# Performance work log

Hardware: AMD Instinct MI355X
Metric: run time of the kernel (lower is better)

## Reference

```python
import jax, jax.numpy as jnp
import numpy as np

UNITS = 256   # wiring.units (state size)
OUT = 64      # wiring.output_dim (motor neurons = last OUT units)


def setup_inputs() -> dict:
    key = jax.random.key(0)
    k_x, k_wi, k_wr, k_mi, k_mr = jax.random.split(key, 5)
    B, L, C = 32, 8192, 128
    x = jax.random.normal(k_x, (B, L, C), dtype=jnp.float32)
    # learned parameters
    W_in = jax.random.normal(k_wi, (C, UNITS), dtype=jnp.float32) * 0.05
    W_rec = jax.random.normal(k_wr, (UNITS, UNITS), dtype=jnp.float32) * 0.05
    b = jnp.zeros((UNITS,), dtype=jnp.float32)
    # fixed sparse wiring masks (sensory adjacency [C,U], recurrent adjacency [U,U])
    M_in = jax.random.bernoulli(k_mi, 0.5, (C, UNITS)).astype(jnp.float32)
    M_rec = jax.random.bernoulli(k_mr, 0.5, (UNITS, UNITS)).astype(jnp.float32)
    return {"x": x, "W_in": W_in, "W_rec": W_rec, "b": b, "M_in": M_in, "M_rec": M_rec}


def reference(x, W_in, W_rec, b, M_in, M_rec):
    # Pre-apply the wiring sparsity masks once (original masks weights each step).
    Wi = W_in * M_in          # [C, U]
    Wr = W_rec * M_rec        # [U, U]
    B = x.shape[0]
    h0 = jnp.zeros((B, UNITS), dtype=x.dtype)
    xT = jnp.swapaxes(x, 0, 1)  # [L, B, C] -> scan over time

    def step(h, xt):
        h_new = jnp.tanh(xt @ Wi + h @ Wr + b)   # wired RNN cell, tanh nonlinearity
        # output_size < state_size: emit only motor neurons (last OUT units)
        return h_new, h_new[:, UNITS - OUT:]

    h_last, ys = jax.lax.scan(step, h0, xT)      # ys: [L, B, OUT]
    readout = jnp.swapaxes(ys, 0, 1)             # [B, L, OUT] (batch_first, return_sequences)
    return readout, h_last
```

## Files before the change

### kernel.cpp

```cpp
#include <hip/hip_runtime.h>
#include <hip/hip_bf16.h>
#include <stdint.h>


#define NB 32
#define SL 8192
#define NC 128
#define NU 256
#define NO 64
#define NK 384
#define GR 64
#define TC 16
#define NCHUNK (SL / TC)

typedef _Float16 h16;
typedef __attribute__((ext_vector_type(2))) _Float16 h16x2;

__device__ __forceinline__ float fdot2f(h16x2 a, h16x2 b, float c) {
#if __has_builtin(__builtin_amdgcn_fdot2)
    return __builtin_amdgcn_fdot2(a, b, c, false);
#else
    return c + (float)a[0] * (float)b[0] + (float)a[1] * (float)b[1];
#endif
}

__device__ __forceinline__ float ftanh(float x) {
#if __has_builtin(__builtin_amdgcn_exp2f) && __has_builtin(__builtin_amdgcn_rcpf)
    float e = __builtin_amdgcn_exp2f(x * 2.8853900817779268f);
    return 1.0f - 2.0f * __builtin_amdgcn_rcpf(e + 1.0f);
#else
    return tanhf(x);
#endif
}

__global__ __launch_bounds__(256, 4) void xw_gemm_kernel(
    const float* __restrict__ x,
    const float* __restrict__ W_in,
    const float* __restrict__ bias,
    const float* __restrict__ M_in,
    h16* __restrict__ xw)
{
    const int u = threadIdx.x;
    const long row0 = (long)blockIdx.x * GR;
    __shared__ h16 xs[GR * NC];

    for (int i = u; i < GR * NC; i += 256)
        xs[i] = (h16)x[row0 * NC + i];

    h16x2 wc[NC / 2];
#pragma unroll
    for (int j = 0; j < NC / 2; ++j) {
        const int k0 = 2 * j, k1 = 2 * j + 1;
        float w0 = W_in[k0 * NU + u] * M_in[k0 * NU + u];
        float w1 = W_in[k1 * NU + u] * M_in[k1 * NU + u];
        h16x2 t; t[0] = (h16)w0; t[1] = (h16)w1;
        wc[j] = t;
    }
    const float bs = bias[u];
    __syncthreads();

    for (int r = 0; r < GR; ++r) {
        const h16x2* xv = (const h16x2*)&xs[r * NC];
        float a0 = bs, a1 = 0.f, a2 = 0.f, a3 = 0.f;
#pragma unroll
        for (int j = 0; j < 16; ++j) {
            a0 = fdot2f(xv[4 * j + 0], wc[4 * j + 0], a0);
            a1 = fdot2f(xv[4 * j + 1], wc[4 * j + 1], a1);
            a2 = fdot2f(xv[4 * j + 2], wc[4 * j + 2], a2);
            a3 = fdot2f(xv[4 * j + 3], wc[4 * j + 3], a3);
        }
        xw[(row0 + r) * NU + u] = (h16)((a0 + a1) + (a2 + a3));
    }
}

__global__ __launch_bounds__(512, 2) void rnn_scan_xw(
    const float* __restrict__ W_rec,
    const float* __restrict__ M_rec,
    const h16* __restrict__ xw,
    float* __restrict__ out)
{
    const int tid  = threadIdx.x;
    const int b    = blockIdx.x;
    const int lane = tid & 63;
    const int wv   = tid >> 6;
    const int u    = (wv << 5) | (lane & 31);
    const int kc   = lane >> 5;
    const int ks   = kc << 7;

    __shared__ __align__(16) h16 vec[2][NU];
    __shared__ __align__(16) h16 xwc[2][TC][NU];

    h16x2 w[64];
#pragma unroll
    for (int j = 0; j < 64; ++j) {
        const int k0 = ks + 2 * j, k1 = k0 + 1;
        float w0 = W_rec[k0 * NU + u] * M_rec[k0 * NU + u];
        float w1 = W_rec[k1 * NU + u] * M_rec[k1 * NU + u];
        h16x2 t; t[0] = (h16)w0; t[1] = (h16)w1;
        w[j] = t;
    }

    const h16* __restrict__ xwb = xw + (long)b * SL * NU;
    float* const outb = out + (long)b * SL * NO;
    const int uo = u - (NU - NO);

    {
        const int4 c0 = ((const int4*)xwb)[tid];
        if (tid < NU) vec[0][tid] = (h16)0.f;
        ((int4*)&xwc[0][0][0])[tid] = c0;
        __syncthreads();
    }

    for (int tc = 0; tc < NCHUNK; ++tc) {
        const int cb = tc & 1;
        const bool havenext = (tc + 1 < NCHUNK);
        int4 creg;
        if (havenext)
            creg = ((const int4*)(xwb + (long)(tc + 1) * TC * NU))[tid];
        float sbuf[TC];

#pragma unroll
        for (int j = 0; j < TC; ++j) {
            const h16x2* v2 = (const h16x2*)(&vec[j & 1][ks]);
            float a0 = 0.f, a1 = 0.f, a2 = 0.f, a3 = 0.f;
#pragma unroll
            for (int q = 0; q < 16; ++q) {
                a0 = fdot2f(v2[4 * q + 0], w[4 * q + 0], a0);
                a1 = fdot2f(v2[4 * q + 1], w[4 * q + 1], a1);
                a2 = fdot2f(v2[4 * q + 2], w[4 * q + 2], a2);
                a3 = fdot2f(v2[4 * q + 3], w[4 * q + 3], a3);
            }
            float s = (a0 + a1) + (a2 + a3);
            if (kc) s += (float)xwc[cb][j][u];
            s += __shfl_xor(s, 32, 64);

            const float hn = ftanh(s);
            if (kc == 0) vec[(j + 1) & 1][u] = (h16)hn;
            sbuf[j] = hn;

            if (j == TC - 1) {
                if (havenext) ((int4*)&xwc[cb ^ 1][0][0])[tid] = creg;
                if (kc == 1 && uo >= 0) {
#pragma unroll
                    for (int jj = 0; jj < TC; ++jj)
                        outb[(long)(tc * TC + jj) * NO + uo] = sbuf[jj];
                }
                if (tc == NCHUNK - 1 && kc == 0)
                    out[(long)NB * SL * NO + (long)b * NU + u] = hn;
            }
            __syncthreads();
        }
    }
}

__global__ __launch_bounds__(1024, 4) void rnn_scan_fallback(
    const float* __restrict__ x,
    const float* __restrict__ W_in,
    const float* __restrict__ W_rec,
    const float* __restrict__ bias,
    const float* __restrict__ M_in,
    const float* __restrict__ M_rec,
    float* __restrict__ out)
{
    const int tid = threadIdx.x;
    const int b   = blockIdx.x;
    const int u   = tid & (NU - 1);
    const int kc  = tid >> 8;
    const int ks  = kc * 96;

    __shared__ __align__(16) h16 vec[NK];
    __shared__ float partial[4][NU];

    h16x2 w[48];
#pragma unroll
    for (int j = 0; j < 48; ++j) {
        const int k0 = ks + 2 * j, k1 = k0 + 1;
        float w0, w1;
        if (k0 < NU) w0 = W_rec[k0 * NU + u] * M_rec[k0 * NU + u];
        else         w0 = W_in[(k0 - NU) * NU + u] * M_in[(k0 - NU) * NU + u];
        if (k1 < NU) w1 = W_rec[k1 * NU + u] * M_rec[k1 * NU + u];
        else         w1 = W_in[(k1 - NU) * NU + u] * M_in[(k1 - NU) * NU + u];
        h16x2 t; t[0] = (h16)w0; t[1] = (h16)w1;
        w[j] = t;
    }
    const float breg = (tid < NU) ? bias[u] : 0.0f;
    const long xbase = (long)b * SL * NC;

    if (tid < NU) vec[tid] = (h16)0.f;
    else if (tid < NU + NC) vec[tid] = (h16)x[xbase + (tid - NU)];
    __syncthreads();

    const bool xthr = (tid >= NU) && (tid < NU + NC);
    for (int t = 0; t < SL; ++t) {
        float xr = 0.f;
        if (xthr && (t + 1 < SL)) xr = x[xbase + (long)(t + 1) * NC + (tid - NU)];

        const h16x2* v2 = (const h16x2*)(&vec[ks]);
        float acc = 0.f;
#pragma unroll
        for (int j = 0; j < 48; ++j) acc = fdot2f(v2[j], w[j], acc);
        partial[kc][u] = acc;
        __syncthreads();

        if (tid < NU) {
            float s = partial[0][u] + partial[1][u] + partial[2][u] + partial[3][u] + breg;
            float hn = ftanh(s);
            vec[u] = (h16)hn;
            if (u >= NU - NO) out[((long)b * SL + t) * NO + (u - (NU - NO))] = hn;
            if (t == SL - 1)  out[(long)NB * SL * NO + (long)b * NU + u] = hn;
        } else if (xthr && (t + 1 < SL)) {
            vec[tid] = (h16)xr;
        }
        __syncthreads();
    }
}

extern "C" void kernel_launch(void* const* d_in, const int* in_sizes, int n_in,
                              void* d_out, int out_size, void* d_ws, size_t ws_size,
                              hipStream_t stream) {
    (void)in_sizes; (void)n_in; (void)out_size;
    const float* x     = (const float*)d_in[0];
    const float* W_in  = (const float*)d_in[1];
    const float* W_rec = (const float*)d_in[2];
    const float* bias  = (const float*)d_in[3];
    const float* M_in  = (const float*)d_in[4];
    const float* M_rec = (const float*)d_in[5];
    float* out = (float*)d_out;

    const size_t xw_bytes = (size_t)NB * SL * NU * sizeof(h16);
    if (ws_size >= xw_bytes) {
        h16* xw = (h16*)d_ws;
        xw_gemm_kernel<<<dim3((NB * SL) / GR), dim3(256), 0, stream>>>(x, W_in, bias, M_in, xw);
        rnn_scan_xw<<<dim3(NB), dim3(512), 0, stream>>>(W_rec, M_rec, xw, out);
    } else {
        rnn_scan_fallback<<<dim3(NB), dim3(1024), 0, stream>>>(x, W_in, W_rec, bias, M_in, M_rec, out);
    }
}
```

Measured before the change: 4.532 ms.

## Register-block four units per thread in recurrent scan with DPP butterfly reduction

Reassigns work in the recurrent scan kernel. Each thread now holds weights for four output units over a 32-wide k-slice, so every hidden-state value read from shared memory feeds four dot products instead of one. The hidden-state vector is stored in a permuted shared-memory order so each thread's slice is contiguous. The eight partial sums per unit are combined with a transpose-style butterfly built on DPP and ds_swizzle instead of a 32-lane shuffle. This is meant to cut LDS traffic and the latency of the cross-lane reduction on the serial per-step critical path, at the cost of more complex indexing and a select-heavy reduction.

Measured after the change: 4.266 ms. 1.06x faster.

```diff
diff --git a/kernel.cpp b/kernel.cpp
--- a/kernel.cpp
+++ b/kernel.cpp
@@ -30,6 +30,28 @@
     return 1.0f - 2.0f * __builtin_amdgcn_rcpf(e + 1.0f);
 #else
     return tanhf(x);
+#endif
+}
+
+__device__ __forceinline__ float xor1f(float x) {
+#if __has_builtin(__builtin_amdgcn_update_dpp)
+    return __int_as_float(__builtin_amdgcn_update_dpp(0, __float_as_int(x), 0xB1, 0xF, 0xF, false));
+#else
+    return __shfl_xor(x, 1, 64);
+#endif
+}
+__device__ __forceinline__ float xor2f(float x) {
+#if __has_builtin(__builtin_amdgcn_update_dpp)
+    return __int_as_float(__builtin_amdgcn_update_dpp(0, __float_as_int(x), 0x4E, 0xF, 0xF, false));
+#else
+    return __shfl_xor(x, 2, 64);
+#endif
+}
+__device__ __forceinline__ float xor4f(float x) {
+#if __has_builtin(__builtin_amdgcn_ds_swizzle)
+    return __int_as_float(__builtin_amdgcn_ds_swizzle(__float_as_int(x), 0x101F));
+#else
+    return __shfl_xor(x, 4, 64);
 #endif
 }
 
@@ -83,26 +105,37 @@
     const int b    = blockIdx.x;
     const int lane = tid & 63;
     const int wv   = tid >> 6;
-    const int u    = (wv << 5) | (lane & 31);
-    const int kc   = lane >> 5;
-    const int ks   = kc << 7;
+    const int kc   = lane & 7;
+    const int g    = lane >> 3;
+    const int G    = (wv << 3) | g;
 
     __shared__ __align__(16) h16 vec[2][NU];
     __shared__ __align__(16) h16 xwc[2][TC][NU];
 
-    h16x2 w[64];
-#pragma unroll
-    for (int j = 0; j < 64; ++j) {
-        const int k0 = ks + 2 * j, k1 = k0 + 1;
-        float w0 = W_rec[k0 * NU + u] * M_rec[k0 * NU + u];
-        float w1 = W_rec[k1 * NU + u] * M_rec[k1 * NU + u];
-        h16x2 t; t[0] = (h16)w0; t[1] = (h16)w1;
-        w[j] = t;
-    }
+    h16x2 w[4][16];
+#pragma unroll
+    for (int j = 0; j < 4; ++j) {
+        const int u = G + 64 * j;
+#pragma unroll
+        for (int q = 0; q < 4; ++q)
+#pragma unroll
+            for (int ep = 0; ep < 4; ++ep) {
+                const int k0 = kc * 32 + q * 8 + 2 * ep;
+                float w0 = W_rec[k0 * NU + u] * M_rec[k0 * NU + u];
+                float w1 = W_rec[(k0 + 1) * NU + u] * M_rec[(k0 + 1) * NU + u];
+                h16x2 t; t[0] = (h16)w0; t[1] = (h16)w1;
+                w[j][q * 4 + ep] = t;
+            }
+    }
+
+    const int  j_of    = 2 * (kc & 1) + ((kc >> 1) & 1);
+    const int  u_mine  = G + 64 * j_of;
+    const bool writer  = (kc < 4);
+    const bool reader  = (kc == 7);
+    const int  pidx    = ((u_mine >> 3) & 3) * 64 + (u_mine >> 5) * 8 + (u_mine & 7);
 
     const h16* __restrict__ xwb = xw + (long)b * SL * NU;
     float* const outb = out + (long)b * SL * NO;
-    const int uo = u - (NU - NO);
 
     {
         const int4 c0 = ((const int4*)xwb)[tid];
@@ -121,32 +154,47 @@
 
 #pragma unroll
         for (int j = 0; j < TC; ++j) {
-            const h16x2* v2 = (const h16x2*)(&vec[j & 1][ks]);
-            float a0 = 0.f, a1 = 0.f, a2 = 0.f, a3 = 0.f;
-#pragma unroll
-            for (int q = 0; q < 16; ++q) {
-                a0 = fdot2f(v2[4 * q + 0], w[4 * q + 0], a0);
-                a1 = fdot2f(v2[4 * q + 1], w[4 * q + 1], a1);
-                a2 = fdot2f(v2[4 * q + 2], w[4 * q + 2], a2);
-                a3 = fdot2f(v2[4 * q + 3], w[4 * q + 3], a3);
+            const float xwv = (float)xwc[cb][j][u_mine];
+
+            const h16x2* v2 = (const h16x2*)&vec[j & 1][0] + (kc << 2);
+            float acc0 = 0.f, acc1 = 0.f, acc2 = 0.f, acc3 = 0.f;
+#pragma unroll
+            for (int q = 0; q < 4; ++q) {
+                const h16x2 x0 = v2[q * 32 + 0], x1 = v2[q * 32 + 1];
+                const h16x2 x2 = v2[q * 32 + 2], x3 = v2[q * 32 + 3];
+                acc0 = fdot2f(x0, w[0][q*4+0], acc0); acc0 = fdot2f(x1, w[0][q*4+1], acc0);
+                acc0 = fdot2f(x2, w[0][q*4+2], acc0); acc0 = fdot2f(x3, w[0][q*4+3], acc0);
+                acc1 = fdot2f(x0, w[1][q*4+0], acc1); acc1 = fdot2f(x1, w[1][q*4+1], acc1);
+                acc1 = fdot2f(x2, w[1][q*4+2], acc1); acc1 = fdot2f(x3, w[1][q*4+3], acc1);
+                acc2 = fdot2f(x0, w[2][q*4+0], acc2); acc2 = fdot2f(x1, w[2][q*4+1], acc2);
+                acc2 = fdot2f(x2, w[2][q*4+2], acc2); acc2 = fdot2f(x3, w[2][q*4+3], acc2);
+                acc3 = fdot2f(x0, w[3][q*4+0], acc3); acc3 = fdot2f(x1, w[3][q*4+1], acc3);
+                acc3 = fdot2f(x2, w[3][q*4+2], acc3); acc3 = fdot2f(x3, w[3][q*4+3], acc3);
             }
-            float s = (a0 + a1) + (a2 + a3);
-            if (kc) s += (float)xwc[cb][j][u];
-            s += __shfl_xor(s, 32, 64);
-
-            const float hn = ftanh(s);
-            if (kc == 0) vec[(j + 1) & 1][u] = (h16)hn;
+
+            const bool o1 = (kc & 1);
+            float s0 = o1 ? acc0 : acc2;
+            float s1 = o1 ? acc1 : acc3;
+            float q0 = (o1 ? acc2 : acc0) + xor1f(s0);
+            float q1 = (o1 ? acc3 : acc1) + xor1f(s1);
+            const bool o2 = (kc & 2);
+            float s2 = o2 ? q0 : q1;
+            float v  = (o2 ? q1 : q0) + xor2f(s2);
+            const float total = v + xor4f(v);
+
+            const float hn = ftanh(total + xwv);
+            if (writer) vec[(j + 1) & 1][pidx] = (h16)hn;
             sbuf[j] = hn;
 
             if (j == TC - 1) {
                 if (havenext) ((int4*)&xwc[cb ^ 1][0][0])[tid] = creg;
-                if (kc == 1 && uo >= 0) {
+                if (reader) {
 #pragma unroll
                     for (int jj = 0; jj < TC; ++jj)
-                        outb[(long)(tc * TC + jj) * NO + uo] = sbuf[jj];
+                        outb[(long)(tc * TC + jj) * NO + G] = sbuf[jj];
                 }
-                if (tc == NCHUNK - 1 && kc == 0)
-                    out[(long)NB * SL * NO + (long)b * NU + u] = hn;
+                if (writer && tc == NCHUNK - 1)
+                    out[(long)NB * SL * NO + (long)b * NU + u_mine] = hn;
             }
             __syncthreads();
         }
```
